# Optimization experiments

Hardware: AMD Instinct MI355X
Metric: run time of the kernel (lower is better)

The kernel has to match this reference:

```python
import jax, jax.numpy as jnp
import numpy as np

BN_EPS = 1e-5


def setup_inputs() -> dict:
    key = jax.random.key(0)
    ks = jax.random.split(key, 8)
    B, C, H, W = 8, 256, 64, 64
    Cqk = C // 8  # query/key channels = out_channels // 8
    x = jax.random.normal(ks[0], (B, C, H, W), dtype=jnp.float32)
    # 1x1 convs == per-pixel matmuls; kaiming-normal-ish scale
    wq = jax.random.normal(ks[1], (Cqk, C), dtype=jnp.float32) * np.sqrt(2.0 / C)
    bq = jnp.zeros((Cqk,), dtype=jnp.float32)
    wk = jax.random.normal(ks[2], (Cqk, C), dtype=jnp.float32) * np.sqrt(2.0 / C)
    bk = jnp.zeros((Cqk,), dtype=jnp.float32)
    wv = jax.random.normal(ks[3], (C, C), dtype=jnp.float32) * np.sqrt(2.0 / C)
    bv = jnp.zeros((C,), dtype=jnp.float32)
    # gamma is initialized to 0 in the original; use a small nonzero value so
    # the attention path actually contributes (and has nontrivial gradients)
    gamma = jnp.full((1,), 0.5, dtype=jnp.float32)
    bn_weight = jnp.ones((C,), dtype=jnp.float32)
    bn_bias = jnp.zeros((C,), dtype=jnp.float32)
    return {"x": x, "wq": wq, "bq": bq, "wk": wk, "bk": bk,
            "wv": wv, "bv": bv, "gamma": gamma,
            "bn_weight": bn_weight, "bn_bias": bn_bias}


def reference(x, wq, bq, wk, bk, wv, bv, gamma, bn_weight, bn_bias):
    B, C, H, W = x.shape
    N = H * W
    xf = x.reshape(B, C, N)  # (B, C, N)
    # 1x1 conv projections as channel matmuls
    q = jnp.einsum('oc,bcn->bno', wq, xf) + bq            # (B, N, Cqk)
    k = jnp.einsum('oc,bcn->bon', wk, xf) + bk[:, None]   # (B, Cqk, N)
    v = jnp.einsum('oc,bcn->bon', wv, xf) + bv[:, None]   # (B, C, N)
    # attention[b, i, j] = softmax_j(q_i . k_j)  -- full N x N matrix
    scores = jnp.einsum('bno,bom->bnm', q, k)             # (B, N, N)
    attn = jax.nn.softmax(scores, axis=2)
    # out[b, c, i] = sum_j v[b, c, j] * attn[b, i, j]
    out = jnp.einsum('bcj,bij->bci', v, attn)             # (B, C, N)
    out = out.reshape(B, C, H, W)
    out = gamma[0] * out + x
    # BatchNorm2d in training mode: batch statistics over (B, H, W)
    mean = jnp.mean(out, axis=(0, 2, 3), keepdims=True)
    var = jnp.var(out, axis=(0, 2, 3), keepdims=True)
    out = (out - mean) * jax.lax.rsqrt(var + BN_EPS)
    out = out * bn_weight[None, :, None, None] + bn_bias[None, :, None, None]
    return jax.nn.relu(out)
```

## Files before the change

### kernel.cpp

```cpp
#include <hip/hip_runtime.h>
#include <stdint.h>

#define B_ 8
#define C_ 256
#define N_ 4096
#define CQK 32
#define VPANEL (C_ * 64)

typedef __attribute__((ext_vector_type(8))) _Float16 f16x8;
typedef __attribute__((ext_vector_type(4))) float f32x4;

__device__ __forceinline__ unsigned short f2bf_rne(float f) {
  unsigned u = __builtin_bit_cast(unsigned, f);
  u += 0x7FFFu + ((u >> 16) & 1u);
  return (unsigned short)(u >> 16);
}

__global__ __launch_bounds__(256) void wconv_kernel(
    const float* __restrict__ wq, const float* __restrict__ wk,
    const float* __restrict__ wv, _Float16* __restrict__ wf)
{
  int idx = blockIdx.x * 256 + threadIdx.x;
  int e = idx * 4;
  int o = e >> 8, c = e & 255;
  const float* src;
  if (o < 32)      src = wq + o * 256 + c;
  else if (o < 64) src = wk + (o - 32) * 256 + c;
  else             src = wv + (o - 64) * 256 + c;
  float4 v = *(const float4*)src;
  _Float16 h[4] = {(_Float16)v.x, (_Float16)v.y, (_Float16)v.z, (_Float16)v.w};
  *(uint2*)(wf + e) = *(uint2*)h;
}

__global__ __launch_bounds__(256, 2) void proj_fused_kernel(
    const float* __restrict__ x, const _Float16* __restrict__ wf,
    const float* __restrict__ bq, const float* __restrict__ bk,
    const float* __restrict__ bv,
    _Float16* __restrict__ qf, _Float16* __restrict__ kf,
    _Float16* __restrict__ vout)
{
  __shared__ float xs[64 * 65];
  __shared__ _Float16 bp[32 * 64 * 8];

  const int t = threadIdx.x, lane = t & 63;
  const int w = t >> 6;
  const int l15 = lane & 15, q4 = lane >> 4;
  const int blk = blockIdx.x;
  const int b  = blk & 7;
  const int nt = blk >> 3;
  const int n0 = nt * 64;
  const int o0w = (w & 1) * 32;
  const int n0w = (w >> 1) * 32;

  for (int ct = 0; ct < 4; ++ct) {
    #pragma unroll
    for (int p = 0; p < 4; ++p) {
      int cc = p * 16 + (t >> 4);
      int nn = (t & 15) * 4;
      float4 v = *(const float4*)(x + ((size_t)(b * C_) + ct * 64 + cc) * N_ + n0 + nn);
      xs[cc * 65 + nn]     = v.x;
      xs[cc * 65 + nn + 1] = v.y;
      xs[cc * 65 + nn + 2] = v.z;
      xs[cc * 65 + nn + 3] = v.w;
    }
    __syncthreads();
    #pragma unroll
    for (int h = 0; h < 2; ++h) {
      int oct = w + h * 4;
      int n = lane;
      _Float16 hh[8];
      #pragma unroll
      for (int j = 0; j < 8; ++j) hh[j] = (_Float16)xs[(oct * 8 + j) * 65 + n];
      *(f16x8*)(bp + (((size_t)(ct * 8 + oct)) * 64 + n) * 8) = *(f16x8*)hh;
    }
    __syncthreads();
  }

  const f32x4 zf = {0.f, 0.f, 0.f, 0.f};
  for (int otile = 0; otile < 5; ++otile) {
    f32x4 acc[2][2];
    #pragma unroll
    for (int a = 0; a < 2; ++a)
      #pragma unroll
      for (int bb = 0; bb < 2; ++bb) acc[a][bb] = zf;

    const _Float16* wbase = wf + (size_t)(otile * 64 + o0w) * 256;

    #pragma unroll
    for (int kc = 0; kc < 8; ++kc) {
      f16x8 af[2], bfr[2];
      #pragma unroll
      for (int ob = 0; ob < 2; ++ob)
        af[ob] = *(const f16x8*)(wbase + (ob * 16 + l15) * 256 + kc * 32 + q4 * 8);
      #pragma unroll
      for (int nb = 0; nb < 2; ++nb)
        bfr[nb] = *(const f16x8*)(bp + (((size_t)(kc * 4 + q4)) * 64 + n0w + nb * 16 + l15) * 8);
      #pragma unroll
      for (int ob = 0; ob < 2; ++ob)
        #pragma unroll
        for (int nb = 0; nb < 2; ++nb)
          acc[ob][nb] = __builtin_amdgcn_mfma_f32_16x16x32_f16(af[ob], bfr[nb], acc[ob][nb], 0, 0, 0);
    }

    if (otile == 0) {
      _Float16* dst = (o0w == 0) ? qf : kf;
      const float* bias = (o0w == 0) ? bq : bk;
      const float qsc = (o0w == 0) ? 1.4426950408889634f : 1.0f;
      #pragma unroll
      for (int ob = 0; ob < 2; ++ob) {
        float4 b4 = *(const float4*)(bias + ob * 16 + q4 * 4);
        #pragma unroll
        for (int nb = 0; nb < 2; ++nb) {
          int pixel = n0 + n0w + nb * 16 + l15;
          _Float16 h[4];
          h[0] = (_Float16)((acc[ob][nb][0] + b4.x) * qsc);
          h[1] = (_Float16)((acc[ob][nb][1] + b4.y) * qsc);
          h[2] = (_Float16)((acc[ob][nb][2] + b4.z) * qsc);
          h[3] = (_Float16)((acc[ob][nb][3] + b4.w) * qsc);
          *(uint2*)(dst + ((size_t)(b * N_) + pixel) * CQK + ob * 16 + q4 * 4) = *(uint2*)h;
        }
      }
    } else {
      int cbase = (otile - 1) * 64 + o0w;
      _Float16* vpan = vout + ((size_t)(b * 64 + nt)) * VPANEL;
      #pragma unroll
      for (int ob = 0; ob < 2; ++ob) {
        float4 b4 = *(const float4*)(bv + cbase + ob * 16 + q4 * 4);
        #pragma unroll
        for (int nb = 0; nb < 2; ++nb) {
          int jj = n0w + nb * 16 + l15;
          #pragma unroll
          for (int r = 0; r < 4; ++r) {
            int c = cbase + ob * 16 + q4 * 4 + r;
            float bval = (r == 0) ? b4.x : (r == 1) ? b4.y : (r == 2) ? b4.z : b4.w;
            vpan[(size_t)c * 64 + jj] = (_Float16)(acc[ob][nb][r] + bval);
          }
        }
      }
    }
  }
}

#define ATTN_BODY(K, BUF) do { \
  f16x8 kx_[8]; \
  { const _Float16* kp_ = kbase + (size_t)(K) * 128 * CQK; \
    _Pragma("unroll") \
    for (int jb = 0; jb < 8; ++jb) kx_[jb] = *(const f16x8*)(kp_ + jb * 16 * CQK); } \
  f16x8 vx_[16]; \
  { const _Float16* vp_ = vbase + (size_t)(K) * 2 * VPANEL; \
    _Pragma("unroll") \
    for (int ks = 0; ks < 4; ++ks) \
      _Pragma("unroll") \
      for (int cb = 0; cb < 4; ++cb) \
        vx_[ks * 4 + cb] = *(const f16x8*)(vp_ + (ks >> 1) * VPANEL + cb * 1024 + (ks & 1) * 32); } \
  f32x4 sv_[8]; \
  _Pragma("unroll") \
  for (int jb = 0; jb < 8; ++jb) \
    sv_[jb] = __builtin_amdgcn_mfma_f32_16x16x32_f16(kx_[jb], qfr, zf, 0, 0, 0); \
  float lm_ = sv_[0][0]; \
  _Pragma("unroll") \
  for (int jb = 0; jb < 8; ++jb) \
    lm_ = fmaxf(lm_, fmaxf(fmaxf(sv_[jb][0], sv_[jb][1]), fmaxf(sv_[jb][2], sv_[jb][3]))); \
  lm_ = fmaxf(lm_, __shfl_xor(lm_, 16)); \
  lm_ = fmaxf(lm_, __shfl_xor(lm_, 32)); \
  bool upd_ = lm_ > mold + 8.0f; \
  unsigned long long bal_ = __ballot(upd_);      \
  float alpha_ = upd_ ? exp2f(mold - lm_) : 1.0f; \
  if (upd_) mold = lm_; \
  float ts_ = 0.f; \
  { char* pb_ = (char*)Plds + (BUF) * 17408 + (w * 16 + l15) * 272 + q4 * 8; \
    _Pragma("unroll") \
    for (int jb = 0; jb < 8; ++jb) { \
      float p0_ = exp2f(sv_[jb][0] - mold), p1_ = exp2f(sv_[jb][1] - mold); \
      float p2_ = exp2f(sv_[jb][2] - mold), p3_ = exp2f(sv_[jb][3] - mold); \
      ts_ += (p0_ + p1_) + (p2_ + p3_); \
      _Float16 h_[4] = {(_Float16)p0_, (_Float16)p1_, (_Float16)p2_, (_Float16)p3_}; \
      *(uint2*)(pb_ + jb * 32) = *(uint2*)h_; } } \
  if (q4 == 0) alphal[(BUF) * 64 + w * 16 + l15] = alpha_; \
  if (lane == 0) flagw[(BUF) * 4 + w] = (bal_ != 0ull) ? 1 : 0; \
  ts_ += __shfl_xor(ts_, 16); \
  ts_ += __shfl_xor(ts_, 32); \
  lrun = lrun * alpha_ + ts_; \
  asm volatile("s_waitcnt lgkmcnt(0)" ::: "memory"); \
  __builtin_amdgcn_sched_barrier(0); \
  __builtin_amdgcn_s_barrier(); \
  asm volatile("" ::: "memory"); \
  { int4 fl_ = *(const int4*)(flagw + (BUF) * 4); \
    if (fl_.x | fl_.y | fl_.z | fl_.w) { \
      _Pragma("unroll") \
      for (int ib = 0; ib < 4; ++ib) { \
        float av_ = alphal[(BUF) * 64 + ib * 16 + l15]; \
        _Pragma("unroll") \
        for (int cb = 0; cb < 4; ++cb) \
          _Pragma("unroll") \
          for (int r = 0; r < 4; ++r) acc[cb][ib][r] *= av_; } } } \
  __builtin_amdgcn_s_setprio(1); \
  _Pragma("unroll") \
  for (int ks = 0; ks < 4; ++ks) { \
    f16x8 pf_[4]; \
    _Pragma("unroll") \
    for (int ib = 0; ib < 4; ++ib) \
      pf_[ib] = *(const f16x8*)((char*)Plds + (BUF) * 17408 + (ib * 16 + l15) * 272 + ks * 64 + q4 * 16); \
    _Pragma("unroll") \
    for (int cb = 0; cb < 4; ++cb) \
      _Pragma("unroll") \
      for (int ib = 0; ib < 4; ++ib) \
        acc[cb][ib] = __builtin_amdgcn_mfma_f32_16x16x32_f16(vx_[ks * 4 + cb], pf_[ib], acc[cb][ib], 0, 0, 0); \
  } \
  __builtin_amdgcn_s_setprio(0); \
} while (0)

__global__ __launch_bounds__(256, 2) void attn_kernel(
    const float* __restrict__ x, const float* __restrict__ gptr,
    const _Float16* __restrict__ qf, const _Float16* __restrict__ kf,
    const _Float16* __restrict__ vf, unsigned short* __restrict__ yout)
{
  __shared__ __align__(16) char smem[35648];
  _Float16* Plds  = (_Float16*)smem;
  float* alphal = (float*)(smem + 34816);
  int*   flagw  = (int*)(smem + 35328);
  float* lrowl  = (float*)(smem + 35360);

  const int t = threadIdx.x, lane = t & 63;
  const int w = t >> 6;
  const int l15 = lane & 15, q4 = lane >> 4;
  const int b  = blockIdx.x & 7;
  const int it = blockIdx.x >> 3;
  const int i0 = it * 64;
  const float gamma = gptr[0];

  const f16x8 qfr = *(const f16x8*)(qf + ((size_t)(b * N_) + i0 + w * 16 + l15) * CQK + q4 * 8);

  const _Float16* kbase = kf + ((size_t)(b * N_) + l15) * CQK + q4 * 8;
  const _Float16* vbase = vf + (size_t)b * (64 * VPANEL)
                             + ((size_t)(w * 64 + l15)) * 64 + q4 * 8;

  f32x4 acc[4][4];
  const f32x4 zf = {0.f, 0.f, 0.f, 0.f};
  #pragma unroll
  for (int a = 0; a < 4; ++a)
    #pragma unroll
    for (int bb = 0; bb < 4; ++bb) acc[a][bb] = zf;

  float mold = -1e30f, lrun = 0.f;

  #pragma unroll 1
  for (int k = 0; k < 32; k += 2) {
    ATTN_BODY(k, 0);
    ATTN_BODY(k + 1, 1);
  }

  if (q4 == 0) lrowl[w * 16 + l15] = lrun;
  __syncthreads();
  #pragma unroll
  for (int ib = 0; ib < 4; ++ib) {
    float linv = 1.0f / lrowl[ib * 16 + l15];
    int i = i0 + ib * 16 + l15;
    #pragma unroll
    for (int cb = 0; cb < 4; ++cb) {
      #pragma unroll
      for (int r = 0; r < 4; ++r) {
        int c = w * 64 + cb * 16 + q4 * 4 + r;
        size_t off = ((size_t)(b * C_) + c) * N_ + i;
        float o = acc[cb][ib][r] * linv;
        yout[off] = f2bf_rne(fmaf(gamma, o, x[off]));
      }
    }
  }
}

__global__ __launch_bounds__(256) void bnstats_kernel(
    const unsigned short* __restrict__ y, float* __restrict__ meanw, float* __restrict__ rstdw)
{
  const int c = blockIdx.x;
  const int t = threadIdx.x;
  float s1 = 0.f, s2 = 0.f;
  for (int b = 0; b < B_; ++b) {
    const unsigned short* p = y + ((size_t)(b * C_ + c)) * N_;
    #pragma unroll
    for (int r = 0; r < 2; ++r) {
      uint4 u = *(const uint4*)(p + r * 2048 + t * 8);
      unsigned uu[4] = {u.x, u.y, u.z, u.w};
      #pragma unroll
      for (int k = 0; k < 4; ++k) {
        float a = __builtin_bit_cast(float, uu[k] << 16);
        float bb = __builtin_bit_cast(float, uu[k] & 0xFFFF0000u);
        s1 += a + bb;
        s2 += a * a + bb * bb;
      }
    }
  }
  __shared__ float r1[256], r2[256];
  r1[t] = s1; r2[t] = s2;
  __syncthreads();
  for (int s = 128; s > 0; s >>= 1) {
    if (t < s) { r1[t] += r1[t + s]; r2[t] += r2[t + s]; }
    __syncthreads();
  }
  if (t == 0) {
    float mean = r1[0] * (1.0f / 32768.0f);
    float var  = r2[0] * (1.0f / 32768.0f) - mean * mean;
    meanw[c] = mean;
    rstdw[c] = rsqrtf(var + 1e-5f);
  }
}

__global__ __launch_bounds__(256) void bnapply_kernel(
    const unsigned short* __restrict__ y, float* __restrict__ out,
    const float* __restrict__ meanw, const float* __restrict__ rstdw,
    const float* __restrict__ bnw, const float* __restrict__ bnb)
{
  size_t idx = (size_t)blockIdx.x * 256 + threadIdx.x;
  size_t el = idx * 8;
  int c = (int)((el >> 12) & 255);
  float sc = bnw[c] * rstdw[c];
  float sh = fmaf(-meanw[c], sc, bnb[c]);
  uint4 u = *(const uint4*)(y + el);
  unsigned uu[4] = {u.x, u.y, u.z, u.w};
  float4 o0, o1;
  float v[8];
  #pragma unroll
  for (int k = 0; k < 4; ++k) {
    v[2 * k]     = __builtin_bit_cast(float, uu[k] << 16);
    v[2 * k + 1] = __builtin_bit_cast(float, uu[k] & 0xFFFF0000u);
  }
  o0.x = fmaxf(fmaf(v[0], sc, sh), 0.f);
  o0.y = fmaxf(fmaf(v[1], sc, sh), 0.f);
  o0.z = fmaxf(fmaf(v[2], sc, sh), 0.f);
  o0.w = fmaxf(fmaf(v[3], sc, sh), 0.f);
  o1.x = fmaxf(fmaf(v[4], sc, sh), 0.f);
  o1.y = fmaxf(fmaf(v[5], sc, sh), 0.f);
  o1.z = fmaxf(fmaf(v[6], sc, sh), 0.f);
  o1.w = fmaxf(fmaf(v[7], sc, sh), 0.f);
  *(float4*)(out + el) = o0;
  *(float4*)(out + el + 4) = o1;
}

extern "C" void kernel_launch(void* const* d_in, const int* in_sizes, int n_in,
                              void* d_out, int out_size, void* d_ws, size_t ws_size,
                              hipStream_t stream)
{
  const float* x   = (const float*)d_in[0];
  const float* wq  = (const float*)d_in[1];
  const float* bq  = (const float*)d_in[2];
  const float* wk  = (const float*)d_in[3];
  const float* bk  = (const float*)d_in[4];
  const float* wv  = (const float*)d_in[5];
  const float* bv  = (const float*)d_in[6];
  const float* gm  = (const float*)d_in[7];
  const float* bnw = (const float*)d_in[8];
  const float* bnb = (const float*)d_in[9];
  float* out = (float*)d_out;

  _Float16* vfp = (_Float16*)((char*)d_out + (size_t)B_ * C_ * N_ * 2);

  char* ws = (char*)d_ws;
  _Float16* qf = (_Float16*)(ws);
  _Float16* kf = (_Float16*)(ws + ((size_t)2 << 20));
  unsigned short* yout = (unsigned short*)(ws + ((size_t)4 << 20));
  _Float16* wf = (_Float16*)(ws + ((size_t)21 << 20));
  float* meanw = (float*)(ws + ((size_t)22 << 20));
  float* rstdw = (float*)(ws + ((size_t)22 << 20) + 4096);

  hipLaunchKernelGGL(wconv_kernel, dim3(80), dim3(256), 0, stream, wq, wk, wv, wf);
  hipLaunchKernelGGL(proj_fused_kernel, dim3(512), dim3(256), 0, stream,
                     x, wf, bq, bk, bv, qf, kf, vfp);
  hipLaunchKernelGGL(attn_kernel, dim3(512), dim3(256), 0, stream,
                     x, gm, qf, kf, vfp, yout);
  hipLaunchKernelGGL(bnstats_kernel, dim3(256), dim3(256), 0, stream,
                     yout, meanw, rstdw);
  hipLaunchKernelGGL(bnapply_kernel, dim3(4096), dim3(256), 0, stream,
                     yout, out, meanw, rstdw, bnw, bnb);
}
```

Baseline: 288.9 us.

## Stage K tiles through double-buffered LDS and use raw v_exp_f32 in softmax

The attention loop used to have each wave load its own K fragments straight from global memory, so all four waves read the same K tile redundantly. Now the block cooperatively loads the next K tile into one of two padded LDS buffers while computing on the current one, and each wave reads its fragments from LDS. The exp2f calls are replaced with the raw v_exp_f32 instruction, and the row max reduction becomes a tree to shorten the dependency chain. LDS use grows to about 56 KB per block, which may limit occupancy against the launch bound of 2 blocks. The exp change also drops denormal handling.

```diff
diff --git a/kernel.cpp b/kernel.cpp
--- a/kernel.cpp
+++ b/kernel.cpp
@@ -14,6 +14,10 @@
   unsigned u = __builtin_bit_cast(unsigned, f);
   u += 0x7FFFu + ((u >> 16) & 1u);
   return (unsigned short)(u >> 16);
+}
+
+__device__ __forceinline__ float fexp2(float x) {
+  float r; asm("v_exp_f32 %0, %1" : "=v"(r) : "v"(x)); return r;
 }
 
 __global__ __launch_bounds__(256) void wconv_kernel(
@@ -142,10 +146,14 @@
 }
 
 #define ATTN_BODY(K, BUF) do { \
-  f16x8 kx_[8]; \
-  { const _Float16* kp_ = kbase + (size_t)(K) * 128 * CQK; \
-    _Pragma("unroll") \
-    for (int jb = 0; jb < 8; ++jb) kx_[jb] = *(const f16x8*)(kp_ + jb * 16 * CQK); } \
+   \
+  f16x8 ks_[2]; \
+  { const _Float16* kg_ = kstage + (size_t)(((K) + 1) & 31) * (128 * CQK); \
+    _Pragma("unroll") \
+    for (int s = 0; s < 2; ++s) { \
+      int idx_ = s * 256 + t; \
+      ks_[s] = *(const f16x8*)(kg_ + (idx_ >> 2) * CQK + (idx_ & 3) * 8); } } \
+   \
   f16x8 vx_[16]; \
   { const _Float16* vp_ = vbase + (size_t)(K) * 2 * VPANEL; \
     _Pragma("unroll") \
@@ -153,29 +161,44 @@
       _Pragma("unroll") \
       for (int cb = 0; cb < 4; ++cb) \
         vx_[ks * 4 + cb] = *(const f16x8*)(vp_ + (ks >> 1) * VPANEL + cb * 1024 + (ks & 1) * 32); } \
+   \
+  f16x8 kx_[8]; \
+  { const _Float16* kl_ = Klds + ((K) & 1) * 5120 + l15 * 40 + q4 * 8; \
+    _Pragma("unroll") \
+    for (int jb = 0; jb < 8; ++jb) kx_[jb] = *(const f16x8*)(kl_ + jb * (16 * 40)); } \
   f32x4 sv_[8]; \
   _Pragma("unroll") \
   for (int jb = 0; jb < 8; ++jb) \
     sv_[jb] = __builtin_amdgcn_mfma_f32_16x16x32_f16(kx_[jb], qfr, zf, 0, 0, 0); \
-  float lm_ = sv_[0][0]; \
+  float pm_[8]; \
   _Pragma("unroll") \
   for (int jb = 0; jb < 8; ++jb) \
-    lm_ = fmaxf(lm_, fmaxf(fmaxf(sv_[jb][0], sv_[jb][1]), fmaxf(sv_[jb][2], sv_[jb][3]))); \
+    pm_[jb] = fmaxf(fmaxf(sv_[jb][0], sv_[jb][1]), fmaxf(sv_[jb][2], sv_[jb][3])); \
+  float ra_ = fmaxf(fmaxf(pm_[0], pm_[1]), pm_[2]); \
+  float rb_ = fmaxf(fmaxf(pm_[3], pm_[4]), pm_[5]); \
+  float rc_ = fmaxf(fmaxf(pm_[6], pm_[7]), ra_); \
+  float lm_ = fmaxf(rb_, rc_); \
   lm_ = fmaxf(lm_, __shfl_xor(lm_, 16)); \
   lm_ = fmaxf(lm_, __shfl_xor(lm_, 32)); \
   bool upd_ = lm_ > mold + 8.0f; \
   unsigned long long bal_ = __ballot(upd_);      \
-  float alpha_ = upd_ ? exp2f(mold - lm_) : 1.0f; \
+  float alpha_ = upd_ ? fexp2(mold - lm_) : 1.0f; \
   if (upd_) mold = lm_; \
   float ts_ = 0.f; \
   { char* pb_ = (char*)Plds + (BUF) * 17408 + (w * 16 + l15) * 272 + q4 * 8; \
     _Pragma("unroll") \
     for (int jb = 0; jb < 8; ++jb) { \
-      float p0_ = exp2f(sv_[jb][0] - mold), p1_ = exp2f(sv_[jb][1] - mold); \
-      float p2_ = exp2f(sv_[jb][2] - mold), p3_ = exp2f(sv_[jb][3] - mold); \
+      float p0_ = fexp2(sv_[jb][0] - mold), p1_ = fexp2(sv_[jb][1] - mold); \
+      float p2_ = fexp2(sv_[jb][2] - mold), p3_ = fexp2(sv_[jb][3] - mold); \
       ts_ += (p0_ + p1_) + (p2_ + p3_); \
       _Float16 h_[4] = {(_Float16)p0_, (_Float16)p1_, (_Float16)p2_, (_Float16)p3_}; \
       *(uint2*)(pb_ + jb * 32) = *(uint2*)h_; } } \
+   \
+  { _Float16* kw_ = Klds + (((K) + 1) & 1) * 5120; \
+    _Pragma("unroll") \
+    for (int s = 0; s < 2; ++s) { \
+      int idx_ = s * 256 + t; \
+      *(f16x8*)(kw_ + (idx_ >> 2) * 40 + (idx_ & 3) * 8) = ks_[s]; } } \
   if (q4 == 0) alphal[(BUF) * 64 + w * 16 + l15] = alpha_; \
   if (lane == 0) flagw[(BUF) * 4 + w] = (bal_ != 0ull) ? 1 : 0; \
   ts_ += __shfl_xor(ts_, 16); \
@@ -215,11 +238,12 @@
     const _Float16* __restrict__ qf, const _Float16* __restrict__ kf,
     const _Float16* __restrict__ vf, unsigned short* __restrict__ yout)
 {
-  __shared__ __align__(16) char smem[35648];
+  __shared__ __align__(16) char smem[56096];
   _Float16* Plds  = (_Float16*)smem;
-  float* alphal = (float*)(smem + 34816);
-  int*   flagw  = (int*)(smem + 35328);
-  float* lrowl  = (float*)(smem + 35360);
+  _Float16* Klds  = (_Float16*)(smem + 34816);
+  float* alphal = (float*)(smem + 55296);
+  int*   flagw  = (int*)(smem + 55808);
+  float* lrowl  = (float*)(smem + 55840);
 
   const int t = threadIdx.x, lane = t & 63;
   const int w = t >> 6;
@@ -231,7 +255,7 @@
 
   const f16x8 qfr = *(const f16x8*)(qf + ((size_t)(b * N_) + i0 + w * 16 + l15) * CQK + q4 * 8);
 
-  const _Float16* kbase = kf + ((size_t)(b * N_) + l15) * CQK + q4 * 8;
+  const _Float16* kstage = kf + (size_t)b * N_ * CQK;
   const _Float16* vbase = vf + (size_t)b * (64 * VPANEL)
                              + ((size_t)(w * 64 + l15)) * 64 + q4 * 8;
 
@@ -243,6 +267,14 @@
     for (int bb = 0; bb < 4; ++bb) acc[a][bb] = zf;
 
   float mold = -1e30f, lrun = 0.f;
+
+  #pragma unroll
+  for (int s = 0; s < 2; ++s) {
+    int idx = s * 256 + t;
+    f16x8 v = *(const f16x8*)(kstage + (idx >> 2) * CQK + (idx & 3) * 8);
+    *(f16x8*)(Klds + (idx >> 2) * 40 + (idx & 3) * 8) = v;
+  }
+  __syncthreads();
 
   #pragma unroll 1
   for (int k = 0; k < 32; k += 2) {
```

Result: faster. 262.8 us (-9.0%).
